# Performance work log

Hardware: AMD Instinct MI355X
Metric: run time of the kernel (lower is better)

Reference implementation:

```python
import jax, jax.numpy as jnp
import numpy as np

B, N, E = 2, 16000, 160000
NDIMS, NMEAS, NMODES = 2, 1, 128
IN_DIM, OUT_DIM, FC_DIM = 3, 1, 128
LAYERS = [64, 64, 64, 64]
INV_MIN, INV_MAX = 0.5, 2.0


def setup_inputs() -> dict:
    key = jax.random.key(0)
    ks = jax.random.split(key, 16)
    L = len(LAYERS) - 1
    C = LAYERS[0]
    scale = 1.0 / (C * C)
    u = lambda k, sh, s: jax.random.uniform(k, sh, jnp.float32, -s, s)
    inp = {}
    inp["x"] = jax.random.normal(ks[0], (B, N, IN_DIM), jnp.float32)
    inp["node_mask"] = jnp.ones((B, N, 1), jnp.int32)
    inp["nodes"] = jax.random.uniform(ks[1], (B, N, NDIMS), jnp.float32)
    inp["node_weights"] = jax.random.uniform(ks[2], (B, N, NMEAS), jnp.float32) / N
    inp["directed_edges"] = jax.random.randint(ks[3], (B, E, 2), 0, N, jnp.int32)
    inp["edge_gradient_weights"] = jax.random.normal(ks[4], (B, E, NDIMS), jnp.float32)
    inp["modes"] = jax.random.normal(ks[5], (NMODES, NDIMS, NMEAS), jnp.float32)
    # scaled_logit(1.0, 0.5, 2.0) = log(0.5/1.0)
    inp["inv_L_scale_latent"] = jnp.full((NDIMS, NMEAS), np.log((1.0 - INV_MIN) / (INV_MAX - 1.0)), jnp.float32)
    inp["fc0_W"] = u(ks[6], (C, IN_DIM), 1.0 / np.sqrt(IN_DIM))
    inp["fc0_b"] = jnp.zeros((C,), jnp.float32)
    inp["weights_c"] = u(ks[7], (L, C, C, NMODES, NMEAS), scale)
    inp["weights_s"] = u(ks[8], (L, C, C, NMODES, NMEAS), scale)
    inp["weights_0"] = u(ks[9], (L, C, C, 1, NMEAS), scale)
    inp["ws_W"] = u(ks[10], (L, C, C), 1.0 / np.sqrt(C))
    inp["ws_b"] = jnp.zeros((L, C), jnp.float32)
    inp["gws_W"] = u(ks[11], (L, C, C * NDIMS), 1.0 / np.sqrt(C * NDIMS))
    inp["gws_b"] = jnp.zeros((L, C), jnp.float32)
    inp["fc1_W"] = u(ks[12], (FC_DIM, C), 1.0 / np.sqrt(C))
    inp["fc1_b"] = jnp.zeros((FC_DIM,), jnp.float32)
    inp["fc2_W"] = u(ks[13], (OUT_DIM, FC_DIM), 1.0 / np.sqrt(FC_DIM))
    inp["fc2_b"] = jnp.zeros((OUT_DIM,), jnp.float32)
    return inp


def _forward(x, nodes, node_weights, edge_gradient_weights, modes, inv_L_scale_latent,
             fc0_W, fc0_b, weights_c, weights_s, weights_0, ws_W, ws_b, gws_W, gws_b,
             fc1_W, fc1_b, fc2_W, fc2_b, directed_edges):
    L = weights_c.shape[0]
    n = x.shape[1]
    # scaled sigmoid of latent inverse length scale
    inv_L = INV_MIN + (INV_MAX - INV_MIN) * jax.nn.sigmoid(inv_L_scale_latent)
    smodes = modes * inv_L  # [K, D, W]
    # Fourier bases over all nodes
    temp = jnp.einsum('bxd,kdw->bxkw', nodes, smodes)  # [B, N, K, W]
    bases_c, bases_s = jnp.cos(temp), jnp.sin(temp)
    bases_0 = jnp.ones(temp.shape[:2] + (1, temp.shape[-1]), temp.dtype)
    wnw = node_weights[:, :, None, :]  # [B, N, 1, W]
    wbases_c, wbases_s, wbases_0 = bases_c * wnw, bases_s * wnw, bases_0 * wnw

    tgt = directed_edges[..., 0]  # [B, E]
    src = directed_edges[..., 1]

    def grad_field(f):  # f: [B, C, N] -> [B, C*D, N]
        ft = jnp.transpose(f, (0, 2, 1))  # [B, N, C]
        f_src = jnp.take_along_axis(ft, src[..., None], axis=1)  # [B, E, C]
        f_tgt = jnp.take_along_axis(ft, tgt[..., None], axis=1)
        diff = f_src - f_tgt
        msg = jnp.einsum('bed,bec->becd', edge_gradient_weights, diff)  # [B, E, C, D]
        msg = msg.reshape(msg.shape[0], msg.shape[1], -1)  # [B, E, C*D]
        seg = jax.vmap(lambda m, t: jax.ops.segment_sum(m, t, num_segments=n))(msg, tgt)
        return jnp.transpose(seg, (0, 2, 1))  # [B, C*D, N]

    # lift: fc0 acts on channel dim
    h = jnp.einsum('oi,bni->bon', fc0_W, x) + fc0_b[None, :, None]  # [B, C, N]

    for i in range(L):
        # spectral conv with explicit bases
        x_c = jnp.einsum('bix,bxkw->bikw', h, wbases_c)
        x_s = -jnp.einsum('bix,bxkw->bikw', h, wbases_s)
        x_0 = jnp.einsum('bix,bxkw->bikw', h, wbases_0)
        f_c = jnp.einsum('bikw,iokw->bokw', x_c, weights_c[i]) - jnp.einsum('bikw,iokw->bokw', x_s, weights_s[i])
        f_s = jnp.einsum('bikw,iokw->bokw', x_s, weights_c[i]) + jnp.einsum('bikw,iokw->bokw', x_c, weights_s[i])
        f_0 = jnp.einsum('bikw,iokw->bokw', x_0, weights_0[i])
        x1 = (jnp.einsum('bokw,bxkw->box', f_0, bases_0)
              + 2 * jnp.einsum('bokw,bxkw->box', f_c, bases_c)
              - 2 * jnp.einsum('bokw,bxkw->box', f_s, bases_s))
        # pointwise linear W
        x2 = jnp.einsum('oi,bin->bon', ws_W[i], h) + ws_b[i][None, :, None]
        # differential operator D: gradient then linear
        x3 = jnp.einsum('oi,bin->bon', gws_W[i], grad_field(h)) + gws_b[i][None, :, None]
        h = x1 + x2 + x3
        if i < L - 1:
            h = jax.nn.gelu(h)

    out = jnp.transpose(h, (0, 2, 1))  # [B, N, C]
    out = jax.nn.gelu(jnp.einsum('oc,bnc->bno', fc1_W, out) + fc1_b)
    out = jnp.einsum('oc,bnc->bno', fc2_W, out) + fc2_b
    return out  # [B, N, out_dim]


def reference(x, node_mask, nodes, node_weights, directed_edges, edge_gradient_weights,
              modes, inv_L_scale_latent, fc0_W, fc0_b, weights_c, weights_s, weights_0,
              ws_W, ws_b, gws_W, gws_b, fc1_W, fc1_b, fc2_W, fc2_b):
    del node_mask  # padding mask; all-ones here, not used in the core math
    return _forward(x, nodes, node_weights, edge_gradient_weights, modes, inv_L_scale_latent,
                    fc0_W, fc0_b, weights_c, weights_s, weights_0, ws_W, ws_b, gws_W, gws_b,
                    fc1_W, fc1_b, fc2_W, fc2_b, directed_edges)
```

## Files before the change

kernel.cpp:

```cpp
#include <hip/hip_runtime.h>
#include <math.h>

#define BB 2
#define NN 16000
#define EE 160000
#define KK 128
#define CC 64
#define LL 3

typedef __attribute__((ext_vector_type(8))) short bf16x8;
typedef __attribute__((ext_vector_type(4))) float f32x4;

__device__ __forceinline__ float gelu_f(float x){
    float x3 = x * x * x;
    return 0.5f * x * (1.f + tanhf(0.7978845608028654f * (x + 0.044715f * x3)));
}
__device__ __forceinline__ ushort f2bf(float f){
    uint u = __float_as_uint(f);
    u += 0x7fff + ((u >> 16) & 1);
    return (ushort)(u >> 16);
}
__device__ __forceinline__ float bf2f(ushort h){ return __uint_as_float(((uint)h) << 16); }
__device__ __forceinline__ void fsplit(float v, ushort &hi, ushort &lo){
    hi = f2bf(v);
    lo = f2bf(v - bf2f(hi));
}
__device__ __forceinline__ uint pk2(ushort a, ushort b){ return (uint)a | ((uint)b << 16); }

__global__ __launch_bounds__(256) void k_bases(
    const float* __restrict__ nodes, const float* __restrict__ modes,
    const float* __restrict__ latent, const float* __restrict__ nw,
    ushort* __restrict__ cbh, ushort* __restrict__ cbl,
    ushort* __restrict__ sbh, ushort* __restrict__ sbl,
    ushort* __restrict__ wTh, ushort* __restrict__ wTl){
    int bid = blockIdx.x;
    int b = bid / 250, x0 = (bid % 250) * 64;
    int t = threadIdx.x;
    __shared__ float sm0[128], sm1[128], nwv[64];
    __shared__ uint tc[64][65], ts[64][65];
    if (t < 128){
        float i0 = 0.5f + 1.5f / (1.f + expf(-latent[0]));
        float i1 = 0.5f + 1.5f / (1.f + expf(-latent[1]));
        sm0[t] = modes[t*2+0] * i0;
        sm1[t] = modes[t*2+1] * i1;
    }
    if (t < 64) nwv[t] = nw[b*NN + x0 + t];
    __syncthreads();
    int xloc = t & 63;
    float n0 = nodes[((size_t)b*NN + x0 + xloc)*2 + 0];
    float n1 = nodes[((size_t)b*NN + x0 + xloc)*2 + 1];
    for (int kh = 0; kh < 2; kh++){
        int kq = t >> 6;
        #pragma unroll
        for (int j = 0; j < 16; j++){
            int kl = kq*16 + j;
            int k = kh*64 + kl;
            float tmp = n0*sm0[k] + n1*sm1[k];
            float sv, cv; sincosf(tmp, &sv, &cv);
            ushort h_, l_;
            fsplit(cv, h_, l_); tc[xloc][kl] = pk2(h_, l_);
            fsplit(sv, h_, l_); ts[xloc][kl] = pk2(h_, l_);
        }
        __syncthreads();
        {
            int q = t >> 6;
            size_t base = ((size_t)b*NN + x0 + xloc)*128 + kh*64 + q*16;
            #pragma unroll
            for (int g2 = 0; g2 < 2; g2++){
                uint u0 = tc[xloc][q*16 + g2*8 + 0], u1 = tc[xloc][q*16 + g2*8 + 1];
                uint u2 = tc[xloc][q*16 + g2*8 + 2], u3 = tc[xloc][q*16 + g2*8 + 3];
                uint u4 = tc[xloc][q*16 + g2*8 + 4], u5 = tc[xloc][q*16 + g2*8 + 5];
                uint u6 = tc[xloc][q*16 + g2*8 + 6], u7 = tc[xloc][q*16 + g2*8 + 7];
                uint4 vh, vl;
                vh.x = pk2((ushort)u0,(ushort)u1); vh.y = pk2((ushort)u2,(ushort)u3);
                vh.z = pk2((ushort)u4,(ushort)u5); vh.w = pk2((ushort)u6,(ushort)u7);
                vl.x = pk2((ushort)(u0>>16),(ushort)(u1>>16)); vl.y = pk2((ushort)(u2>>16),(ushort)(u3>>16));
                vl.z = pk2((ushort)(u4>>16),(ushort)(u5>>16)); vl.w = pk2((ushort)(u6>>16),(ushort)(u7>>16));
                *(uint4*)&cbh[base + g2*8] = vh;
                *(uint4*)&cbl[base + g2*8] = vl;
                u0 = ts[xloc][q*16 + g2*8 + 0]; u1 = ts[xloc][q*16 + g2*8 + 1];
                u2 = ts[xloc][q*16 + g2*8 + 2]; u3 = ts[xloc][q*16 + g2*8 + 3];
                u4 = ts[xloc][q*16 + g2*8 + 4]; u5 = ts[xloc][q*16 + g2*8 + 5];
                u6 = ts[xloc][q*16 + g2*8 + 6]; u7 = ts[xloc][q*16 + g2*8 + 7];
                vh.x = pk2((ushort)u0,(ushort)u1); vh.y = pk2((ushort)u2,(ushort)u3);
                vh.z = pk2((ushort)u4,(ushort)u5); vh.w = pk2((ushort)u6,(ushort)u7);
                vl.x = pk2((ushort)(u0>>16),(ushort)(u1>>16)); vl.y = pk2((ushort)(u2>>16),(ushort)(u3>>16));
                vl.z = pk2((ushort)(u4>>16),(ushort)(u5>>16)); vl.w = pk2((ushort)(u6>>16),(ushort)(u7>>16));
                *(uint4*)&sbh[base + g2*8] = vh;
                *(uint4*)&sbl[base + g2*8] = vl;
            }
        }
        {
            int k = t & 63, g = t >> 6;
            int kgc = kh*64 + k;
            int kgs = 128 + kh*64 + k;
            ushort hc[16], lc[16], hs[16], ls[16];
            #pragma unroll
            for (int j = 0; j < 16; j++){
                int xx = g*16 + j;
                float wgt = nwv[xx];
                uint uc = tc[xx][k], us = ts[xx][k];
                float vc = (bf2f((ushort)uc) + bf2f((ushort)(uc>>16))) * wgt;
                float vs = (bf2f((ushort)us) + bf2f((ushort)(us>>16))) * wgt;
                fsplit(vc, hc[j], lc[j]);
                fsplit(vs, hs[j], ls[j]);
            }
            size_t wbc = ((size_t)b*256 + kgc)*16000 + x0 + g*16;
            size_t wbs = ((size_t)b*256 + kgs)*16000 + x0 + g*16;
            uint4 v;
            v.x = pk2(hc[0],hc[1]); v.y = pk2(hc[2],hc[3]); v.z = pk2(hc[4],hc[5]); v.w = pk2(hc[6],hc[7]);
            *(uint4*)&wTh[wbc] = v;
            v.x = pk2(hc[8],hc[9]); v.y = pk2(hc[10],hc[11]); v.z = pk2(hc[12],hc[13]); v.w = pk2(hc[14],hc[15]);
            *(uint4*)&wTh[wbc + 8] = v;
            v.x = pk2(lc[0],lc[1]); v.y = pk2(lc[2],lc[3]); v.z = pk2(lc[4],lc[5]); v.w = pk2(lc[6],lc[7]);
            *(uint4*)&wTl[wbc] = v;
            v.x = pk2(lc[8],lc[9]); v.y = pk2(lc[10],lc[11]); v.z = pk2(lc[12],lc[13]); v.w = pk2(lc[14],lc[15]);
            *(uint4*)&wTl[wbc + 8] = v;
            v.x = pk2(hs[0],hs[1]); v.y = pk2(hs[2],hs[3]); v.z = pk2(hs[4],hs[5]); v.w = pk2(hs[6],hs[7]);
            *(uint4*)&wTh[wbs] = v;
            v.x = pk2(hs[8],hs[9]); v.y = pk2(hs[10],hs[11]); v.z = pk2(hs[12],hs[13]); v.w = pk2(hs[14],hs[15]);
            *(uint4*)&wTh[wbs + 8] = v;
            v.x = pk2(ls[0],ls[1]); v.y = pk2(ls[2],ls[3]); v.z = pk2(ls[4],ls[5]); v.w = pk2(ls[6],ls[7]);
            *(uint4*)&wTl[wbs] = v;
            v.x = pk2(ls[8],ls[9]); v.y = pk2(ls[10],ls[11]); v.z = pk2(ls[12],ls[13]); v.w = pk2(ls[14],ls[15]);
            *(uint4*)&wTl[wbs + 8] = v;
        }
        __syncthreads();
    }
}

__device__ __forceinline__ void write_h_outputs(
    const float* ot, const float* nws, int b, int s, int x0, int t, int doAux,
    float* __restrict__ hx, ushort* __restrict__ hxh, ushort* __restrict__ hxl,
    ushort* __restrict__ hwh, ushort* __restrict__ hwl, float* __restrict__ part0){
    {
        int xl = t >> 1, half = t & 1;
        size_t gb = ((size_t)b*NN + x0 + xl)*64 + half*32;
        const float* row = &ot[xl*68 + half*32];
        #pragma unroll
        for (int j = 0; j < 8; j++){
            float4 v; v.x = row[j*4]; v.y = row[j*4+1]; v.z = row[j*4+2]; v.w = row[j*4+3];
            *(float4*)&hx[gb + j*4] = v;
        }
        if (doAux){
            #pragma unroll
            for (int q = 0; q < 4; q++){
                ushort h_[8], l_[8];
                #pragma unroll
                for (int j = 0; j < 8; j++) fsplit(row[q*8 + j], h_[j], l_[j]);
                uint4 vh, vl;
                vh.x = pk2(h_[0],h_[1]); vh.y = pk2(h_[2],h_[3]); vh.z = pk2(h_[4],h_[5]); vh.w = pk2(h_[6],h_[7]);
                vl.x = pk2(l_[0],l_[1]); vl.y = pk2(l_[2],l_[3]); vl.z = pk2(l_[4],l_[5]); vl.w = pk2(l_[6],l_[7]);
                *(uint4*)&hxh[gb + q*8] = vh;
                *(uint4*)&hxl[gb + q*8] = vl;
            }
        }
    }
    if (doAux){
        int i = t & 63, g = t >> 6;
        float a = 0.f;
        #pragma unroll
        for (int rep = 0; rep < 4; rep++){
            int xs = g*32 + rep*8;
            ushort h_[8], l_[8];
            #pragma unroll
            for (int j = 0; j < 8; j++){
                float v = ot[(xs + j)*68 + i] * nws[xs + j];
                a += v;
                fsplit(v, h_[j], l_[j]);
            }
            uint4 vh, vl;
            vh.x = pk2(h_[0],h_[1]); vh.y = pk2(h_[2],h_[3]); vh.z = pk2(h_[4],h_[5]); vh.w = pk2(h_[6],h_[7]);
            vl.x = pk2(l_[0],l_[1]); vl.y = pk2(l_[2],l_[3]); vl.z = pk2(l_[4],l_[5]); vl.w = pk2(l_[6],l_[7]);
            size_t wb = (size_t)(b*64 + i)*16000 + x0 + xs;
            *(uint4*)&hwh[wb] = vh;
            *(uint4*)&hwl[wb] = vl;
        }
        part0[((size_t)(b*125 + s)*4 + g)*64 + i] = a;
    }
}

__global__ __launch_bounds__(256) void k_fc0(
    const float* __restrict__ x, const float* __restrict__ W,
    const float* __restrict__ bb, const float* __restrict__ nw,
    float* __restrict__ hx, ushort* __restrict__ hxh, ushort* __restrict__ hxl,
    ushort* __restrict__ hwh, ushort* __restrict__ hwl, float* __restrict__ part0){
    int bid = blockIdx.x;
    int b = bid / 125, s = bid % 125;
    int x0 = s * 128;
    int t = threadIdx.x;
    __shared__ float ot[128*68];
    __shared__ float nws[128];
    __shared__ float Wf[192], bf_[64];
    if (t < 192) Wf[t] = W[t];
    if (t < 64) bf_[t] = bb[t];
    if (t < 128) nws[t] = nw[b*NN + x0 + t];
    __syncthreads();
    {
        int xl = t >> 1, half = t & 1;
        float v0 = x[((size_t)b*NN + x0 + xl)*3 + 0];
        float v1 = x[((size_t)b*NN + x0 + xl)*3 + 1];
        float v2 = x[((size_t)b*NN + x0 + xl)*3 + 2];
        #pragma unroll
        for (int j = 0; j < 32; j++){
            int o = half*32 + j;
            ot[xl*68 + o] = Wf[o*3]*v0 + Wf[o*3+1]*v1 + Wf[o*3+2]*v2 + bf_[o];
        }
    }
    __syncthreads();
    write_h_outputs(ot, nws, b, s, x0, t, 1, hx, hxh, hxl, hwh, hwl, part0);
}

__global__ __launch_bounds__(256) void csr_hist(
    const int* __restrict__ edges, int* __restrict__ cnt){
    int idx = blockIdx.x * 256 + threadIdx.x;
    if (idx >= BB*EE) return;
    int b = idx / EE;
    int tgt = edges[(size_t)idx*2];
    atomicAdd(&cnt[b*NN + tgt], 1);
}

__global__ __launch_bounds__(1024) void csr_scan(
    const int* __restrict__ cnt, int* __restrict__ rowptr, int* __restrict__ cursor){
    int b = blockIdx.x;
    int t = threadIdx.x;
    __shared__ int lds[1024];
    int base = t * 16;
    int v[16];
    int run = 0;
    #pragma unroll
    for (int j = 0; j < 16; j++){
        int n = base + j;
        int c = (n < NN) ? cnt[b*NN + n] : 0;
        v[j] = run;
        run += c;
    }
    lds[t] = run;
    __syncthreads();
    for (int off = 1; off < 1024; off <<= 1){
        int xv = (t >= off) ? lds[t-off] : 0;
        __syncthreads();
        lds[t] += xv;
        __syncthreads();
    }
    int toff = lds[t] - run;
    #pragma unroll
    for (int j = 0; j < 16; j++){
        int n = base + j;
        if (n < NN){
            int p = toff + v[j];
            rowptr[b*(NN+1) + n] = p;
            cursor[b*NN + n] = p;
        }
    }
    if (t == 1023) rowptr[b*(NN+1) + NN] = lds[1023];
}

__global__ __launch_bounds__(256) void csr_fill(
    const int* __restrict__ edges, const float* __restrict__ egw,
    int* __restrict__ cursor, int* __restrict__ insrc, float2* __restrict__ inw){
    int idx = blockIdx.x * 256 + threadIdx.x;
    if (idx >= BB*EE) return;
    int b = idx / EE;
    int tgt = edges[(size_t)idx*2];
    int src = edges[(size_t)idx*2 + 1];
    int pos = atomicAdd(&cursor[b*NN + tgt], 1);
    insrc[(size_t)b*EE + pos] = src;
    const float2 wv = *(const float2*)&egw[(size_t)idx*2];
    inw[(size_t)b*EE + pos] = wv;
}

__global__ __launch_bounds__(256) void k1_fwd(
    const ushort* __restrict__ hwH, const ushort* __restrict__ hwL,
    const ushort* __restrict__ wTH, const ushort* __restrict__ wTL,
    float* __restrict__ part){
    int bid = blockIdx.x;
    int b = bid / 250, s = bid % 250;
    int x0 = s * 64;
    int t = threadIdx.x, l = t & 63, w = t >> 6;
    __shared__ __align__(16) ushort Bh[128*64], Bl[128*64];
    f32x4 acc[16] = {};
    bf16x8 Ah[2], Al[2];
    int i = w*16 + (l & 15);
    #pragma unroll
    for (int ks = 0; ks < 2; ks++){
        size_t ab = (size_t)(b*64 + i)*16000 + x0 + ks*32 + ((l >> 4) * 8);
        Ah[ks] = *reinterpret_cast<const bf16x8*>(&hwH[ab]);
        Al[ks] = *reinterpret_cast<const bf16x8*>(&hwL[ab]);
    }
    for (int p = 0; p < 2; p++){
        #pragma unroll
        for (int it = 0; it < 4; it++){
            int u = it*256 + t;
            int kloc = u >> 3, q = u & 7;
            size_t g = ((size_t)(b*256 + p*128 + kloc))*16000 + x0 + q*8;
            uint4 vh = *(const uint4*)&wTH[g];
            uint4 vl = *(const uint4*)&wTL[g];
            int ldsb = kloc*128 + ((q*16) ^ ((kloc & 7) << 4));
            *(uint4*)&Bh[ldsb >> 1] = vh;
            *(uint4*)&Bl[ldsb >> 1] = vl;
        }
        __syncthreads();
        #pragma unroll
        for (int kt = 0; kt < 8; kt++){
            int kcol = kt*16 + (l & 15);
            int ai = p*8 + kt;
            #pragma unroll
            for (int ks = 0; ks < 2; ks++){
                int boff = kcol*128 + (((ks*64) + ((l >> 4) * 16)) ^ ((kcol & 7) << 4));
                bf16x8 bh = *reinterpret_cast<const bf16x8*>(&Bh[boff >> 1]);
                bf16x8 bl = *reinterpret_cast<const bf16x8*>(&Bl[boff >> 1]);
                acc[ai] = __builtin_amdgcn_mfma_f32_16x16x32_bf16(Ah[ks], bh, acc[ai], 0, 0, 0);
                acc[ai] = __builtin_amdgcn_mfma_f32_16x16x32_bf16(Ah[ks], bl, acc[ai], 0, 0, 0);
                acc[ai] = __builtin_amdgcn_mfma_f32_16x16x32_bf16(Al[ks], bh, acc[ai], 0, 0, 0);
            }
        }
        __syncthreads();
    }
    size_t pb = (size_t)(b*250 + s) * 64 * 256;
    #pragma unroll
    for (int nt = 0; nt < 16; nt++){
        #pragma unroll
        for (int r = 0; r < 4; r++){
            int irow = w*16 + (l >> 4)*4 + r;
            part[pb + (size_t)irow*256 + nt*16 + (l & 15)] = acc[nt][r];
        }
    }
}

__global__ __launch_bounds__(512) void k1_reduce(
    const float* __restrict__ part, float* __restrict__ Sc, float* __restrict__ Ss){
    int b = blockIdx.x >> 6, i = blockIdx.x & 63;
    int t = threadIdx.x;
    int c = t & 255, sh = t >> 8;
    float a0=0,a1=0,a2=0,a3=0;
    int j = sh;
    for (; j + 6 < 250; j += 8){
        a0 += part[((size_t)(b*250 + j    )*64 + i)*256 + c];
        a1 += part[((size_t)(b*250 + j + 2)*64 + i)*256 + c];
        a2 += part[((size_t)(b*250 + j + 4)*64 + i)*256 + c];
        a3 += part[((size_t)(b*250 + j + 6)*64 + i)*256 + c];
    }
    for (; j < 250; j += 2)
        a0 += part[((size_t)(b*250 + j)*64 + i)*256 + c];
    float sum = (a0+a1)+(a2+a3);
    __shared__ float r2[256];
    if (sh) r2[c] = sum;
    __syncthreads();
    if (!sh){
        sum += r2[c];
        if (c < 128) Sc[(size_t)(b*64 + i)*128 + c] = sum;
        else         Ss[(size_t)(b*64 + i)*128 + (c - 128)] = sum;
    }
}

__global__ __launch_bounds__(256) void k2_mix(
    const float* __restrict__ Sc, const float* __restrict__ Ss,
    const float* __restrict__ part0,
    const float* __restrict__ wc, const float* __restrict__ wsp,
    const float* __restrict__ w0,
    const float* __restrict__ wsb, const float* __restrict__ gwsb,
    const float* __restrict__ wsW, const float* __restrict__ gwsW,
    ushort* __restrict__ WbH, ushort* __restrict__ WbL,
    float* __restrict__ bias, int l){
    int b = blockIdx.x >> 6, o = blockIdx.x & 63;
    int t = threadIdx.x;
    __shared__ float fc2s[2][128], fs2s[2][128];
    __shared__ float red[64];
    if (t < 64){
        float x0 = 0.f;
        for (int s2 = 0; s2 < 500; s2++) x0 += part0[(size_t)(b*500 + s2)*64 + t];
        red[t] = x0 * w0[((size_t)l*CC + t)*CC + o];
    }
    int k = t & 127, hf = t >> 7;
    float fc = 0.f, fs = 0.f;
    for (int i = hf*32; i < hf*32 + 32; i++){
        float sc = Sc[(size_t)(b*CC + i)*KK + k];
        float ss = Ss[(size_t)(b*CC + i)*KK + k];
        size_t wi = (((size_t)l*CC + i)*CC + o)*KK + k;
        float a = wc[wi], bb2 = wsp[wi];
        fc += sc*a + ss*bb2;
        fs += sc*bb2 - ss*a;
    }
    fc2s[hf][k] = fc; fs2s[hf][k] = fs;
    __syncthreads();
    size_t wb = (size_t)(b*CC + o) * 448;
    if (t < 128){
        float FC = fc2s[0][t] + fc2s[1][t];
        float FS = fs2s[0][t] + fs2s[1][t];
        ushort h_, l_;
        fsplit(2.f*FC, h_, l_);
        WbH[wb + t] = h_; WbL[wb + t] = l_;
        fsplit(-2.f*FS, h_, l_);
        WbH[wb + 128 + t] = h_; WbL[wb + 128 + t] = l_;
    }
    if (t < 192){
        float v = (t < 64) ? wsW[((size_t)l*CC + o)*CC + t]
                           : gwsW[((size_t)l*CC + o)*128 + (t - 64)];
        ushort h_, l_; fsplit(v, h_, l_);
        WbH[wb + 256 + t] = h_; WbL[wb + 256 + t] = l_;
    }
    if (t == 0){
        float f0 = 0.f;
        for (int i = 0; i < 64; i++) f0 += red[i];
        bias[b*CC + o] = f0 + wsb[l*CC + o] + gwsb[l*CC + o];
    }
}

__global__ __launch_bounds__(256) void k_grad(
    const float* __restrict__ h, const int* __restrict__ rowptr,
    const int* __restrict__ insrc, const float2* __restrict__ inw,
    ushort* __restrict__ segh, ushort* __restrict__ segl){
    int bid = blockIdx.x;
    int b = bid / 2000, n0 = (bid % 2000) * 8;
    int w = threadIdx.x >> 6, c = threadIdx.x & 63;
    const float*  hb  = h + (size_t)b*NN*CC;
    const int*    isb = insrc + (size_t)b*EE;
    const float2* iwb = inw + (size_t)b*EE;
    #pragma unroll
    for (int g = 0; g < 2; g++){
        int n = n0 + w*2 + g;
        float hn = hb[(size_t)n*CC + c];
        int p0 = rowptr[b*(NN+1) + n];
        int p1 = rowptr[b*(NN+1) + n + 1];
        float a0 = 0.f, a1 = 0.f;
        int p = p0;
        for (; p + 4 <= p1; p += 4){
            int s0 = isb[p], s1 = isb[p+1], s2 = isb[p+2], s3 = isb[p+3];
            float2 w0 = iwb[p], w1 = iwb[p+1], w2 = iwb[p+2], w3 = iwb[p+3];
            float d0 = hb[(size_t)s0*CC + c] - hn;
            float d1 = hb[(size_t)s1*CC + c] - hn;
            float d2 = hb[(size_t)s2*CC + c] - hn;
            float d3 = hb[(size_t)s3*CC + c] - hn;
            a0 += w0.x*d0 + w1.x*d1 + w2.x*d2 + w3.x*d3;
            a1 += w0.y*d0 + w1.y*d1 + w2.y*d2 + w3.y*d3;
        }
        for (; p < p1; p++){
            int sx = isb[p]; float2 ww = iwb[p];
            float d = hb[(size_t)sx*CC + c] - hn;
            a0 += ww.x*d; a1 += ww.y*d;
        }
        ushort h0_, l0_, h1_, l1_;
        fsplit(a0, h0_, l0_);
        fsplit(a1, h1_, l1_);
        size_t sb2 = ((size_t)b*NN + n)*128 + 2*c;
        *(uint*)&segh[sb2] = pk2(h0_, h1_);
        *(uint*)&segl[sb2] = pk2(l0_, l1_);
    }
}

__global__ __launch_bounds__(256) void k3_gemm(
    const ushort* __restrict__ WbH, const ushort* __restrict__ WbL,
    const float* __restrict__ bias,
    const ushort* __restrict__ cbh, const ushort* __restrict__ cbl,
    const ushort* __restrict__ sbh, const ushort* __restrict__ sbl,
    const ushort* __restrict__ hxh, const ushort* __restrict__ hxl,
    const ushort* __restrict__ sgh, const ushort* __restrict__ sgl,
    const float* __restrict__ nw,
    float* __restrict__ hxO, ushort* __restrict__ hxhO, ushort* __restrict__ hxlO,
    ushort* __restrict__ hwhO, ushort* __restrict__ hwlO, float* __restrict__ part0,
    int doAux){
    int bid = blockIdx.x;
    int b = bid / 125, s = bid % 125, x0 = s * 128;
    int t = threadIdx.x, l = t & 63, w = t >> 6;
    __shared__ __align__(16) char smem[34816];
    ushort* Vh = (ushort*)smem;
    ushort* Vl = Vh + 8192;
    __shared__ float nws[128];
    if (t < 128) nws[t] = nw[b*NN + x0 + t];
    f32x4 acc[8] = {};
    int o = w*16 + (l & 15);
    for (int cc = 0; cc < 7; cc++){
        const ushort *srcH, *srcL; int rl, co;
        switch (cc){
            case 0:  srcH = cbh; srcL = cbl; rl = 128; co = 0;  break;
            case 1:  srcH = cbh; srcL = cbl; rl = 128; co = 64; break;
            case 2:  srcH = sbh; srcL = sbl; rl = 128; co = 0;  break;
            case 3:  srcH = sbh; srcL = sbl; rl = 128; co = 64; break;
            case 4:  srcH = hxh; srcL = hxl; rl = 64;  co = 0;  break;
            case 5:  srcH = sgh; srcL = sgl; rl = 128; co = 0;  break;
            default: srcH = sgh; srcL = sgl; rl = 128; co = 64; break;
        }
        __syncthreads();
        #pragma unroll
        for (int it = 0; it < 4; it++){
            int u = it*256 + t;
            int xl2 = u >> 3, q = u & 7;
            size_t g = (size_t)(b*NN + x0 + xl2)*rl + co + q*8;
            uint4 vh = *(const uint4*)&srcH[g];
            uint4 vl2 = *(const uint4*)&srcL[g];
            int ldsb = xl2*128 + ((q*16) ^ ((xl2 & 7) << 4));
            *(uint4*)&Vh[ldsb >> 1] = vh;
            *(uint4*)&Vl[ldsb >> 1] = vl2;
        }
        __syncthreads();
        bf16x8 Ah[2], Al[2];
        #pragma unroll
        for (int ks = 0; ks < 2; ks++){
            size_t ab = (size_t)(b*64 + o)*448 + cc*64 + ks*32 + ((l >> 4) * 8);
            Ah[ks] = *reinterpret_cast<const bf16x8*>(&WbH[ab]);
            Al[ks] = *reinterpret_cast<const bf16x8*>(&WbL[ab]);
        }
        #pragma unroll
        for (int nt = 0; nt < 8; nt++){
            int xc = nt*16 + (l & 15);
            #pragma unroll
            for (int ks = 0; ks < 2; ks++){
                int boff = xc*128 + (((ks*64) + ((l >> 4) * 16)) ^ ((xc & 7) << 4));
                bf16x8 bh = *reinterpret_cast<const bf16x8*>(&Vh[boff >> 1]);
                bf16x8 bl = *reinterpret_cast<const bf16x8*>(&Vl[boff >> 1]);
                acc[nt] = __builtin_amdgcn_mfma_f32_16x16x32_bf16(Ah[ks], bh, acc[nt], 0, 0, 0);
                acc[nt] = __builtin_amdgcn_mfma_f32_16x16x32_bf16(Ah[ks], bl, acc[nt], 0, 0, 0);
                acc[nt] = __builtin_amdgcn_mfma_f32_16x16x32_bf16(Al[ks], bh, acc[nt], 0, 0, 0);
            }
        }
    }
    __syncthreads();
    float* ot = (float*)smem;
    float bv[4];
    #pragma unroll
    for (int r = 0; r < 4; r++) bv[r] = bias[b*64 + w*16 + (l >> 4)*4 + r];
    #pragma unroll
    for (int nt = 0; nt < 8; nt++){
        int xc = nt*16 + (l & 15);
        #pragma unroll
        for (int r = 0; r < 4; r++){
            float v = acc[nt][r] + bv[r];
            if (doAux) v = gelu_f(v);
            ot[xc*68 + (w*16 + (l >> 4)*4 + r)] = v;
        }
    }
    __syncthreads();
    write_h_outputs(ot, nws, b, s, x0, t, doAux, hxO, hxhO, hxlO, hwhO, hwlO, part0);
}

__global__ __launch_bounds__(256) void k_head(
    const float* __restrict__ h, const float* __restrict__ W1,
    const float* __restrict__ b1, const float* __restrict__ W2,
    const float* __restrict__ b2, float* __restrict__ out){
    int bid = blockIdx.x;
    int b = bid / 250, n0 = (bid % 250) * 64;
    int t = threadIdx.x, w = t >> 6, f = t & 63;
    __shared__ float Wl[128][65];
    #pragma unroll
    for (int r = 0; r < 8; r++){
        int u = r*256 + t;
        int ff = u >> 4, cq = u & 15;
        float4 v = *(const float4*)&W1[ff*64 + cq*4];
        Wl[ff][cq*4+0] = v.x; Wl[ff][cq*4+1] = v.y;
        Wl[ff][cq*4+2] = v.z; Wl[ff][cq*4+3] = v.w;
    }
    __syncthreads();
    float w2a = W2[f], w2b = W2[64+f];
    float b1a = b1[f], b1b = b1[64+f];
    float b2v = b2[0];
    for (int g = 0; g < 16; g++){
        int n = n0 + w*16 + g;
        float hv = h[((size_t)b*NN + n)*CC + f];
        float a1 = b1a, a2 = b1b;
        #pragma unroll
        for (int c2 = 0; c2 < 64; c2++){
            float xv = __shfl(hv, c2, 64);
            a1 += Wl[f][c2] * xv;
            a2 += Wl[64+f][c2] * xv;
        }
        float p = gelu_f(a1)*w2a + gelu_f(a2)*w2b;
        for (int off = 32; off; off >>= 1) p += __shfl_down(p, off, 64);
        if (f == 0) out[(size_t)b*NN + n] = p + b2v;
    }
}

extern "C" void kernel_launch(void* const* d_in, const int* in_sizes, int n_in,
                              void* d_out, int out_size, void* d_ws, size_t ws_size,
                              hipStream_t stream){
    const float* x_in  = (const float*)d_in[0];
    const float* nodes = (const float*)d_in[2];
    const float* nw    = (const float*)d_in[3];
    const int*   edges = (const int*)d_in[4];
    const float* egw   = (const float*)d_in[5];
    const float* modes = (const float*)d_in[6];
    const float* latent= (const float*)d_in[7];
    const float* fc0W  = (const float*)d_in[8];
    const float* fc0b  = (const float*)d_in[9];
    const float* wc    = (const float*)d_in[10];
    const float* wsp   = (const float*)d_in[11];
    const float* w0    = (const float*)d_in[12];
    const float* wsW   = (const float*)d_in[13];
    const float* wsb   = (const float*)d_in[14];
    const float* gwsW  = (const float*)d_in[15];
    const float* gwsb  = (const float*)d_in[16];
    const float* fc1W  = (const float*)d_in[17];
    const float* fc1b  = (const float*)d_in[18];
    const float* fc2W  = (const float*)d_in[19];
    const float* fc2b  = (const float*)d_in[20];
    float* out = (float*)d_out;

    char* wsbase = (char*)d_ws;
    size_t off = 0;
    auto alloc = [&](size_t bytes) -> void* {
        void* p = wsbase + off;
        off += (bytes + 255) & ~(size_t)255;
        return p;
    };
    ushort* cbh = (ushort*)alloc((size_t)BB*NN*128*2);
    ushort* cbl = (ushort*)alloc((size_t)BB*NN*128*2);
    ushort* sbh = (ushort*)alloc((size_t)BB*NN*128*2);
    ushort* sbl = (ushort*)alloc((size_t)BB*NN*128*2);
    ushort* wTh = (ushort*)alloc((size_t)BB*256*NN*2);
    ushort* wTl = (ushort*)alloc((size_t)BB*256*NN*2);
    float*  hx[2];  ushort* hxh[2]; ushort* hxl[2]; ushort* hwh[2]; ushort* hwl[2];
    for (int i = 0; i < 2; i++){
        hx[i]  = (float*) alloc((size_t)BB*NN*64*4);
        hxh[i] = (ushort*)alloc((size_t)BB*NN*64*2);
        hxl[i] = (ushort*)alloc((size_t)BB*NN*64*2);
        hwh[i] = (ushort*)alloc((size_t)BB*64*NN*2);
        hwl[i] = (ushort*)alloc((size_t)BB*64*NN*2);
    }
    ushort* segh = (ushort*)alloc((size_t)BB*NN*128*2);
    ushort* segl = (ushort*)alloc((size_t)BB*NN*128*2);
    float*  part = (float*) alloc((size_t)BB*250*64*256*4);
    float*  part0= (float*) alloc((size_t)BB*125*4*64*4);
    float*  Sc   = (float*) alloc((size_t)BB*64*128*4);
    float*  Ss   = (float*) alloc((size_t)BB*64*128*4);
    ushort* WbH  = (ushort*)alloc((size_t)BB*64*448*2);
    ushort* WbL  = (ushort*)alloc((size_t)BB*64*448*2);
    float*  bias = (float*) alloc((size_t)BB*64*4);
    int*   cnt   = (int*)   alloc((size_t)BB*NN*4);
    int*   rowptr= (int*)   alloc((size_t)BB*(NN+4)*4);
    int*   cursor= (int*)   alloc((size_t)BB*NN*4);
    int*   insrc = (int*)   alloc((size_t)BB*EE*4);
    float2* inw  = (float2*)alloc((size_t)BB*EE*8);

    k_bases<<<BB*250, 256, 0, stream>>>(nodes, modes, latent, nw,
                                        cbh, cbl, sbh, sbl, wTh, wTl);
    k_fc0<<<BB*125, 256, 0, stream>>>(x_in, fc0W, fc0b, nw,
                                      hx[0], hxh[0], hxl[0], hwh[0], hwl[0], part0);

    hipMemsetAsync(cnt, 0, (size_t)BB*NN*4, stream);
    csr_hist<<<(BB*EE+255)/256, 256, 0, stream>>>(edges, cnt);
    csr_scan<<<BB, 1024, 0, stream>>>(cnt, rowptr, cursor);
    csr_fill<<<(BB*EE+255)/256, 256, 0, stream>>>(edges, egw, cursor, insrc, inw);

    int cur = 0;
    for (int l = 0; l < LL; l++){
        int nxt = cur ^ 1;
        int doAux = (l < LL-1) ? 1 : 0;
        k1_fwd<<<BB*250, 256, 0, stream>>>(hwh[cur], hwl[cur], wTh, wTl, part);
        k1_reduce<<<BB*64, 512, 0, stream>>>(part, Sc, Ss);
        k2_mix<<<BB*64, 256, 0, stream>>>(Sc, Ss, part0, wc, wsp, w0, wsb, gwsb,
                                          wsW, gwsW, WbH, WbL, bias, l);
        k_grad<<<BB*2000, 256, 0, stream>>>(hx[cur], rowptr, insrc, inw, segh, segl);
        k3_gemm<<<BB*125, 256, 0, stream>>>(WbH, WbL, bias,
                                            cbh, cbl, sbh, sbl,
                                            hxh[cur], hxl[cur], segh, segl, nw,
                                            hx[nxt], hxh[nxt], hxl[nxt],
                                            hwh[nxt], hwl[nxt], part0, doAux);
        cur = nxt;
    }
    k_head<<<BB*250, 256, 0, stream>>>(hx[cur], fc1W, fc1b, fc2W, fc2b, out);
    (void)in_sizes; (void)n_in; (void)out_size; (void)ws_size; (void)segh; (void)segl;
}
```

Baseline: 509.2 us.

## Widen spectral GEMM tile, regrid reductions, vectorize gradient gather

k1_fwd now uses 512-thread blocks covering 128 nodes. The two wave groups' accumulators are summed through LDS, which halves the partial-sum buffer and the work left for k1_reduce. k1_reduce is regridded to match, and k2_mix spreads the part0 reduction across all threads instead of one 64-thread loop. k_grad processes 4 channels per thread with float4 gathers and 16-byte stores, and handles 32 nodes per block. The trade-off is larger LDS use (64 KB), which lowers occupancy in k1_fwd, and fewer blocks in k_grad.

```diff
diff --git a/kernel.cpp b/kernel.cpp
--- a/kernel.cpp
+++ b/kernel.cpp
@@ -270,33 +270,37 @@
     inw[(size_t)b*EE + pos] = wv;
 }
 
-__global__ __launch_bounds__(256) void k1_fwd(
+__global__ __launch_bounds__(512) void k1_fwd(
     const ushort* __restrict__ hwH, const ushort* __restrict__ hwL,
     const ushort* __restrict__ wTH, const ushort* __restrict__ wTL,
     float* __restrict__ part){
     int bid = blockIdx.x;
-    int b = bid / 250, s = bid % 250;
-    int x0 = s * 64;
+    int b = bid / 125, s = bid % 125;
+    int x0 = s * 128;
     int t = threadIdx.x, l = t & 63, w = t >> 6;
-    __shared__ __align__(16) ushort Bh[128*64], Bl[128*64];
+    int wi = w & 3, xh = w >> 2;
+    __shared__ __align__(16) char smem[65536];
+    ushort* Bh = (ushort*)smem;
+    ushort* Bl = Bh + 128*128;
     f32x4 acc[16] = {};
     bf16x8 Ah[2], Al[2];
-    int i = w*16 + (l & 15);
+    int i = wi*16 + (l & 15);
     #pragma unroll
     for (int ks = 0; ks < 2; ks++){
-        size_t ab = (size_t)(b*64 + i)*16000 + x0 + ks*32 + ((l >> 4) * 8);
+        size_t ab = (size_t)(b*64 + i)*16000 + x0 + xh*64 + ks*32 + ((l >> 4) * 8);
         Ah[ks] = *reinterpret_cast<const bf16x8*>(&hwH[ab]);
         Al[ks] = *reinterpret_cast<const bf16x8*>(&hwL[ab]);
     }
     for (int p = 0; p < 2; p++){
+        if (p) __syncthreads();
         #pragma unroll
         for (int it = 0; it < 4; it++){
-            int u = it*256 + t;
-            int kloc = u >> 3, q = u & 7;
+            int u = it*512 + t;
+            int kloc = u >> 4, q = u & 15;
             size_t g = ((size_t)(b*256 + p*128 + kloc))*16000 + x0 + q*8;
             uint4 vh = *(const uint4*)&wTH[g];
             uint4 vl = *(const uint4*)&wTL[g];
-            int ldsb = kloc*128 + ((q*16) ^ ((kloc & 7) << 4));
+            int ldsb = kloc*256 + ((q*16) ^ ((kloc & 7) << 4));
             *(uint4*)&Bh[ldsb >> 1] = vh;
             *(uint4*)&Bl[ldsb >> 1] = vl;
         }
@@ -307,7 +311,7 @@
             int ai = p*8 + kt;
             #pragma unroll
             for (int ks = 0; ks < 2; ks++){
-                int boff = kcol*128 + (((ks*64) + ((l >> 4) * 16)) ^ ((kcol & 7) << 4));
+                int boff = kcol*256 + ((xh*128 + ks*64 + ((l >> 4) * 16)) ^ ((kcol & 7) << 4));
                 bf16x8 bh = *reinterpret_cast<const bf16x8*>(&Bh[boff >> 1]);
                 bf16x8 bl = *reinterpret_cast<const bf16x8*>(&Bl[boff >> 1]);
                 acc[ai] = __builtin_amdgcn_mfma_f32_16x16x32_bf16(Ah[ks], bh, acc[ai], 0, 0, 0);
@@ -315,40 +319,53 @@
                 acc[ai] = __builtin_amdgcn_mfma_f32_16x16x32_bf16(Al[ks], bh, acc[ai], 0, 0, 0);
             }
         }
-        __syncthreads();
-    }
-    size_t pb = (size_t)(b*250 + s) * 64 * 256;
-    #pragma unroll
-    for (int nt = 0; nt < 16; nt++){
-        #pragma unroll
-        for (int r = 0; r < 4; r++){
-            int irow = w*16 + (l >> 4)*4 + r;
-            part[pb + (size_t)irow*256 + nt*16 + (l & 15)] = acc[nt][r];
-        }
-    }
-}
-
-__global__ __launch_bounds__(512) void k1_reduce(
+    }
+    __syncthreads();
+    float* red = (float*)smem;
+    if (t >= 256){
+        int row = t - 256;
+        #pragma unroll
+        for (int nt = 0; nt < 16; nt++)
+            *(f32x4*)&red[row*64 + ((nt*4) ^ ((row & 7) << 2))] = acc[nt];
+    }
+    __syncthreads();
+    if (t < 256){
+        size_t pb = (size_t)(b*125 + s) * 64 * 256;
+        #pragma unroll
+        for (int nt = 0; nt < 16; nt++){
+            f32x4 o = *(f32x4*)&red[t*64 + ((nt*4) ^ ((t & 7) << 2))];
+            #pragma unroll
+            for (int r = 0; r < 4; r++){
+                int irow = wi*16 + (l >> 4)*4 + r;
+                part[pb + (size_t)irow*256 + nt*16 + (l & 15)] = acc[nt][r] + o[r];
+            }
+        }
+    }
+}
+
+__global__ __launch_bounds__(256) void k1_reduce(
     const float* __restrict__ part, float* __restrict__ Sc, float* __restrict__ Ss){
-    int b = blockIdx.x >> 6, i = blockIdx.x & 63;
+    int bid = blockIdx.x;
+    int b = bid >> 7, rr = bid & 127;
+    int i = rr >> 1, kh = rr & 1;
     int t = threadIdx.x;
-    int c = t & 255, sh = t >> 8;
+    int c = kh*128 + (t & 127), sh = t >> 7;
+    const float* pb = part + ((size_t)b*125*64 + i)*256 + c;
     float a0=0,a1=0,a2=0,a3=0;
     int j = sh;
-    for (; j + 6 < 250; j += 8){
-        a0 += part[((size_t)(b*250 + j    )*64 + i)*256 + c];
-        a1 += part[((size_t)(b*250 + j + 2)*64 + i)*256 + c];
-        a2 += part[((size_t)(b*250 + j + 4)*64 + i)*256 + c];
-        a3 += part[((size_t)(b*250 + j + 6)*64 + i)*256 + c];
-    }
-    for (; j < 250; j += 2)
-        a0 += part[((size_t)(b*250 + j)*64 + i)*256 + c];
+    for (; j + 6 < 125; j += 8){
+        a0 += pb[(size_t)(j    )*16384];
+        a1 += pb[(size_t)(j + 2)*16384];
+        a2 += pb[(size_t)(j + 4)*16384];
+        a3 += pb[(size_t)(j + 6)*16384];
+    }
+    for (; j < 125; j += 2) a0 += pb[(size_t)j*16384];
     float sum = (a0+a1)+(a2+a3);
-    __shared__ float r2[256];
-    if (sh) r2[c] = sum;
+    __shared__ float r2[128];
+    if (sh) r2[t & 127] = sum;
     __syncthreads();
     if (!sh){
-        sum += r2[c];
+        sum += r2[t & 127];
         if (c < 128) Sc[(size_t)(b*64 + i)*128 + c] = sum;
         else         Ss[(size_t)(b*64 + i)*128 + (c - 128)] = sum;
     }
@@ -366,11 +383,14 @@
     int b = blockIdx.x >> 6, o = blockIdx.x & 63;
     int t = threadIdx.x;
     __shared__ float fc2s[2][128], fs2s[2][128];
+    __shared__ float redp[4][64];
     __shared__ float red[64];
-    if (t < 64){
-        float x0 = 0.f;
-        for (int s2 = 0; s2 < 500; s2++) x0 += part0[(size_t)(b*500 + s2)*64 + t];
-        red[t] = x0 * w0[((size_t)l*CC + t)*CC + o];
+    {
+        int i = t & 63, grp = t >> 6;
+        float a = 0.f;
+        for (int s2 = grp; s2 < 500; s2 += 4)
+            a += part0[(size_t)(b*500 + s2)*64 + i];
+        redp[grp][i] = a;
     }
     int k = t & 127, hf = t >> 7;
     float fc = 0.f, fs = 0.f;
@@ -384,6 +404,8 @@
     }
     fc2s[hf][k] = fc; fs2s[hf][k] = fs;
     __syncthreads();
+    if (t < 64)
+        red[t] = (redp[0][t]+redp[1][t]+redp[2][t]+redp[3][t]) * w0[((size_t)l*CC + t)*CC + o];
     size_t wb = (size_t)(b*CC + o) * 448;
     if (t < 128){
         float FC = fc2s[0][t] + fc2s[1][t];
@@ -394,12 +416,23 @@
         fsplit(-2.f*FS, h_, l_);
         WbH[wb + 128 + t] = h_; WbL[wb + 128 + t] = l_;
     }
-    if (t < 192){
-        float v = (t < 64) ? wsW[((size_t)l*CC + o)*CC + t]
-                           : gwsW[((size_t)l*CC + o)*128 + (t - 64)];
+    if (t >= 128 && t < 320 - 128){
+        int q = t - 128;
+        float v = wsW[((size_t)l*CC + o)*CC + q];
         ushort h_, l_; fsplit(v, h_, l_);
-        WbH[wb + 256 + t] = h_; WbL[wb + 256 + t] = l_;
-    }
+        WbH[wb + 256 + q] = h_; WbL[wb + 256 + q] = l_;
+    }
+    if (t >= 64 && t < 128){
+    }
+    {
+        if (t >= 128){
+            int q = t - 128;
+            float v = gwsW[((size_t)l*CC + o)*128 + q];
+            ushort h_, l_; fsplit(v, h_, l_);
+            WbH[wb + 320 + q] = h_; WbL[wb + 320 + q] = l_;
+        }
+    }
+    __syncthreads();
     if (t == 0){
         float f0 = 0.f;
         for (int i = 0; i < 64; i++) f0 += red[i];
@@ -412,40 +445,54 @@
     const int* __restrict__ insrc, const float2* __restrict__ inw,
     ushort* __restrict__ segh, ushort* __restrict__ segl){
     int bid = blockIdx.x;
-    int b = bid / 2000, n0 = (bid % 2000) * 8;
-    int w = threadIdx.x >> 6, c = threadIdx.x & 63;
+    int b = bid / 500, n0 = (bid % 500) * 32;
+    int slot = threadIdx.x >> 4, c4 = threadIdx.x & 15;
     const float*  hb  = h + (size_t)b*NN*CC;
     const int*    isb = insrc + (size_t)b*EE;
     const float2* iwb = inw + (size_t)b*EE;
+    const int* rp = rowptr + b*(NN+1);
     #pragma unroll
     for (int g = 0; g < 2; g++){
-        int n = n0 + w*2 + g;
-        float hn = hb[(size_t)n*CC + c];
-        int p0 = rowptr[b*(NN+1) + n];
-        int p1 = rowptr[b*(NN+1) + n + 1];
-        float a0 = 0.f, a1 = 0.f;
+        int n = n0 + slot + 16*g;
+        float4 hn = *(const float4*)&hb[(size_t)n*64 + c4*4];
+        int p0 = rp[n], p1 = rp[n+1];
+        float4 aw = {0.f,0.f,0.f,0.f}, av = {0.f,0.f,0.f,0.f};
         int p = p0;
-        for (; p + 4 <= p1; p += 4){
-            int s0 = isb[p], s1 = isb[p+1], s2 = isb[p+2], s3 = isb[p+3];
-            float2 w0 = iwb[p], w1 = iwb[p+1], w2 = iwb[p+2], w3 = iwb[p+3];
-            float d0 = hb[(size_t)s0*CC + c] - hn;
-            float d1 = hb[(size_t)s1*CC + c] - hn;
-            float d2 = hb[(size_t)s2*CC + c] - hn;
-            float d3 = hb[(size_t)s3*CC + c] - hn;
-            a0 += w0.x*d0 + w1.x*d1 + w2.x*d2 + w3.x*d3;
-            a1 += w0.y*d0 + w1.y*d1 + w2.y*d2 + w3.y*d3;
-        }
-        for (; p < p1; p++){
-            int sx = isb[p]; float2 ww = iwb[p];
-            float d = hb[(size_t)sx*CC + c] - hn;
-            a0 += ww.x*d; a1 += ww.y*d;
-        }
-        ushort h0_, l0_, h1_, l1_;
-        fsplit(a0, h0_, l0_);
-        fsplit(a1, h1_, l1_);
-        size_t sb2 = ((size_t)b*NN + n)*128 + 2*c;
-        *(uint*)&segh[sb2] = pk2(h0_, h1_);
-        *(uint*)&segl[sb2] = pk2(l0_, l1_);
+        for (; p + 2 <= p1; p += 2){
+            int s0 = isb[p], s1 = isb[p+1];
+            float2 w0 = iwb[p], w1 = iwb[p+1];
+            float4 d0 = *(const float4*)&hb[(size_t)s0*64 + c4*4];
+            float4 d1 = *(const float4*)&hb[(size_t)s1*64 + c4*4];
+            d0.x -= hn.x; d0.y -= hn.y; d0.z -= hn.z; d0.w -= hn.w;
+            d1.x -= hn.x; d1.y -= hn.y; d1.z -= hn.z; d1.w -= hn.w;
+            aw.x += w0.x*d0.x + w1.x*d1.x; av.x += w0.y*d0.x + w1.y*d1.x;
+            aw.y += w0.x*d0.y + w1.x*d1.y; av.y += w0.y*d0.y + w1.y*d1.y;
+            aw.z += w0.x*d0.z + w1.x*d1.z; av.z += w0.y*d0.z + w1.y*d1.z;
+            aw.w += w0.x*d0.w + w1.x*d1.w; av.w += w0.y*d0.w + w1.y*d1.w;
+        }
+        if (p < p1){
+            int s0 = isb[p];
+            float2 w0 = iwb[p];
+            float4 d0 = *(const float4*)&hb[(size_t)s0*64 + c4*4];
+            d0.x -= hn.x; d0.y -= hn.y; d0.z -= hn.z; d0.w -= hn.w;
+            aw.x += w0.x*d0.x; av.x += w0.y*d0.x;
+            aw.y += w0.x*d0.y; av.y += w0.y*d0.y;
+            aw.z += w0.x*d0.z; av.z += w0.y*d0.z;
+            aw.w += w0.x*d0.w; av.w += w0.y*d0.w;
+        }
+        ushort h_[8], l_[8];
+        fsplit(aw.x, h_[0], l_[0]); fsplit(av.x, h_[1], l_[1]);
+        fsplit(aw.y, h_[2], l_[2]); fsplit(av.y, h_[3], l_[3]);
+        fsplit(aw.z, h_[4], l_[4]); fsplit(av.z, h_[5], l_[5]);
+        fsplit(aw.w, h_[6], l_[6]); fsplit(av.w, h_[7], l_[7]);
+        uint4 vh, vl;
+        vh.x = pk2(h_[0],h_[1]); vh.y = pk2(h_[2],h_[3]);
+        vh.z = pk2(h_[4],h_[5]); vh.w = pk2(h_[6],h_[7]);
+        vl.x = pk2(l_[0],l_[1]); vl.y = pk2(l_[2],l_[3]);
+        vl.z = pk2(l_[4],l_[5]); vl.w = pk2(l_[6],l_[7]);
+        size_t sb2 = ((size_t)b*NN + n)*128 + c4*8;
+        *(uint4*)&segh[sb2] = vh;
+        *(uint4*)&segl[sb2] = vl;
     }
 }
 
@@ -618,7 +665,7 @@
     }
     ushort* segh = (ushort*)alloc((size_t)BB*NN*128*2);
     ushort* segl = (ushort*)alloc((size_t)BB*NN*128*2);
-    float*  part = (float*) alloc((size_t)BB*250*64*256*4);
+    float*  part = (float*) alloc((size_t)BB*125*64*256*4);
     float*  part0= (float*) alloc((size_t)BB*125*4*64*4);
     float*  Sc   = (float*) alloc((size_t)BB*64*128*4);
     float*  Ss   = (float*) alloc((size_t)BB*64*128*4);
@@ -645,11 +692,11 @@
     for (int l = 0; l < LL; l++){
         int nxt = cur ^ 1;
         int doAux = (l < LL-1) ? 1 : 0;
-        k1_fwd<<<BB*250, 256, 0, stream>>>(hwh[cur], hwl[cur], wTh, wTl, part);
-        k1_reduce<<<BB*64, 512, 0, stream>>>(part, Sc, Ss);
+        k1_fwd<<<BB*125, 512, 0, stream>>>(hwh[cur], hwl[cur], wTh, wTl, part);
+        k1_reduce<<<BB*128, 256, 0, stream>>>(part, Sc, Ss);
         k2_mix<<<BB*64, 256, 0, stream>>>(Sc, Ss, part0, wc, wsp, w0, wsb, gwsb,
                                           wsW, gwsW, WbH, WbL, bias, l);
-        k_grad<<<BB*2000, 256, 0, stream>>>(hx[cur], rowptr, insrc, inw, segh, segl);
+        k_grad<<<BB*500, 256, 0, stream>>>(hx[cur], rowptr, insrc, inw, segh, segl);
         k3_gemm<<<BB*125, 256, 0, stream>>>(WbH, WbL, bias,
                                             cbh, cbl, sbh, sbl,
                                             hxh[cur], hxl[cur], segh, segl, nw,
@@ -658,5 +705,5 @@
         cur = nxt;
     }
     k_head<<<BB*250, 256, 0, stream>>>(hx[cur], fc1W, fc1b, fc2W, fc2b, out);
-    (void)in_sizes; (void)n_in; (void)out_size; (void)ws_size; (void)segh; (void)segl;
-}
+    (void)in_sizes; (void)n_in; (void)out_size; (void)ws_size;
+}
```

Result: slower. 561.1 us (+10.2%).
